# Optimization experiments

Measured on AMD Instinct MI355X. Metric: run time of the kernel, lower is better.

## Reference

```python
import jax, jax.numpy as jnp
import numpy as np

N = 200_000          # active voxels
CIN, COUT = 64, 128  # in_filters, out_filters
GRID = (32, 480, 480)  # sparse spatial shape (D, H, W)
NEG_SLOPE = 0.01     # nn.LeakyReLU default
EPS = 1e-5           # BatchNorm1d default


def _build_nbrs():
    """Build rulebook-style neighbor tables for the two submanifold kernels.

    Returns nbr31 [9, N] for kernel (3,1,3) and nbr13 [9, N] for kernel (1,3,3).
    Entry == N means 'no active neighbor' (maps to a zero pad row).
    """
    rng = np.random.default_rng(0)
    prod = GRID[0] * GRID[1] * GRID[2]
    lin = rng.choice(prod, size=N, replace=False)
    z, y, x = np.unravel_index(lin, GRID)
    lut = np.full(prod, N, dtype=np.int64)
    lut[lin] = np.arange(N)

    def nbrs(offsets):
        out = np.full((len(offsets), N), N, dtype=np.int32)
        for k, (dz, dy, dx) in enumerate(offsets):
            zz, yy, xx = z + dz, y + dy, x + dx
            valid = ((zz >= 0) & (zz < GRID[0]) & (yy >= 0) & (yy < GRID[1])
                     & (xx >= 0) & (xx < GRID[2]))
            l2 = (zz * GRID[1] + yy) * GRID[2] + xx
            out[k, valid] = lut[l2[valid]].astype(np.int32)
        return out

    off31 = [(dz, 0, dx) for dz in (-1, 0, 1) for dx in (-1, 0, 1)]  # (3,1,3)
    off13 = [(0, dy, dx) for dy in (-1, 0, 1) for dx in (-1, 0, 1)]  # (1,3,3)
    return nbrs(off31), nbrs(off13)


def setup_inputs() -> dict:
    key = jax.random.key(0)
    ks = jax.random.split(key, 5)
    nbr31, nbr13 = _build_nbrs()
    s_in = (2.0 / (9 * CIN)) ** 0.5
    s_out = (2.0 / (9 * COUT)) ** 0.5
    ones = jnp.ones((COUT,), jnp.float32)
    zeros = jnp.zeros((COUT,), jnp.float32)
    return {
        "feats": jax.random.normal(ks[0], (N, CIN), jnp.float32),
        "W1": jax.random.normal(ks[1], (9, CIN, COUT), jnp.float32) * s_in,
        "W1_2": jax.random.normal(ks[2], (9, COUT, COUT), jnp.float32) * s_out,
        "W2": jax.random.normal(ks[3], (9, CIN, COUT), jnp.float32) * s_in,
        "W3": jax.random.normal(ks[4], (9, COUT, COUT), jnp.float32) * s_out,
        "g0": ones, "b0": zeros,      # bn0  (init: weight=1, bias=0)
        "g0_2": ones, "b0_2": zeros,  # bn0_2
        "g1": ones, "b1": zeros,      # bn1
        "g2": ones, "b2": zeros,      # bn2
        "nbr31": jnp.asarray(nbr31),
        "nbr13": jnp.asarray(nbr13),
    }


def _subm_conv(f, W, nbr):
    # f [N, Cin], W [9, Cin, Cout], nbr [9, N] -> [N, Cout]
    fp = jnp.concatenate([f, jnp.zeros((1, f.shape[1]), f.dtype)], axis=0)
    g = fp[nbr]  # gather: [9, N, Cin]
    return jnp.einsum("knc,kcd->nd", g, W)


def _lrelu(f):
    return jnp.where(f >= 0, f, NEG_SLOPE * f)


def _bn(f, gamma, beta):
    # BatchNorm1d training-mode batch stats (biased variance) over voxel dim
    m = jnp.mean(f, axis=0)
    v = jnp.mean(jnp.square(f), axis=0) - m * m
    return (f - m) * jax.lax.rsqrt(v + EPS) * gamma + beta


def reference(feats, W1, W1_2, W2, W3, g0, b0, g0_2, b0_2, g1, b1, g2, b2,
              nbr31, nbr13):
    shortcut = _bn(_lrelu(_subm_conv(feats, W1, nbr31)), g0, b0)
    shortcut = _bn(_lrelu(_subm_conv(shortcut, W1_2, nbr13)), g0_2, b0_2)
    resA = _bn(_lrelu(_subm_conv(feats, W2, nbr13)), g1, b1)
    resA = _bn(_lrelu(_subm_conv(resA, W3, nbr31)), g2, b2)
    return resA + shortcut
```

## Files before the change

kernel.cpp:

```cpp
#include <hip/hip_runtime.h>

#define NV 200000
#define NCH 782
#define PCAP 32
#define CG 3125
#define PN 3907
#define RB1 123

typedef __attribute__((ext_vector_type(8))) short sh8;
typedef __attribute__((ext_vector_type(4))) float f32x4;
typedef __attribute__((ext_vector_type(2))) unsigned int u32x2;

__device__ inline unsigned short f2bf(float f) {
  unsigned int u = __builtin_bit_cast(unsigned int, f);
  u += 0x7FFFu + ((u >> 16) & 1u);
  return (unsigned short)(u >> 16);
}
__device__ inline float bf2f(unsigned short h) {
  unsigned int u = ((unsigned int)h) << 16;
  return __builtin_bit_cast(float, u);
}
__device__ inline float lrelu(float v) { return v >= 0.f ? v : 0.01f * v; }

__global__ __launch_bounds__(256) void prep_k(
    const float* __restrict__ W1, const float* __restrict__ W12,
    const float* __restrict__ W2, const float* __restrict__ W3,
    unsigned short* __restrict__ T1, unsigned short* __restrict__ T12,
    unsigned short* __restrict__ T2, unsigned short* __restrict__ T3,
    const int* __restrict__ nbr31, const int* __restrict__ nbr13,
    int2* __restrict__ pairs, int* __restrict__ cc) {
  __shared__ unsigned short lt[64 * 130];
  __shared__ int base_s[4];
  int bx = blockIdx.x;
  const int tid = threadIdx.x;
  if (bx < 36) {
    const float* src;
    unsigned short* dst;
    int cin, k;
    if (bx < 9) { src = W1; dst = T1; cin = 64; k = bx; }
    else if (bx < 18) { src = W2; dst = T2; cin = 64; k = bx - 9; }
    else if (bx < 27) { src = W12; dst = T12; cin = 128; k = bx - 18; }
    else { src = W3; dst = T3; cin = 128; k = bx - 27; }
    src += (size_t)k * cin * 128;
    dst += (size_t)k * 128 * cin;
    const int cmask = cin - 1;
    const int csh = (cin == 64) ? 6 : 7;
    for (int h = 0; h < 2; ++h) {
      if (h) __syncthreads();
      const int tot = cin * 64;
      for (int e = tid; e < tot; e += 256) {
        const int c = e >> 6, dd = e & 63;
        lt[dd * 130 + c] = f2bf(src[c * 128 + h * 64 + dd]);
      }
      __syncthreads();
      for (int o = tid; o < tot; o += 256) {
        const int dl = o >> csh, c = o & cmask;
        dst[(size_t)(h * 64 + dl) * cin + c] = lt[dl * 130 + c];
      }
    }
    return;
  }
  bx -= 36;
  const int slot = bx / NCH, chunk = bx % NCH;
  const int table = slot >> 3, kk = slot & 7;
  const int k = kk + (kk >= 4);
  const int* nb = (table ? nbr13 : nbr31) + (size_t)k * NV;
  const int lane = tid & 63, wv = tid >> 6;
  const int n = chunk * 256 + tid;
  const int val = (n < NV) ? nb[n] : NV;
  const bool valid = (val != NV);
  const unsigned long long m = __ballot(valid);
  const int loff = __popcll(m & ((1ull << lane) - 1ull));
  if (lane == 0) base_s[wv] = __popcll(m);
  __syncthreads();
  int wbase = 0;
  for (int w = 0; w < wv; ++w) wbase += base_s[w];
  int2* pw = pairs + (size_t)(slot * NCH + chunk) * PCAP;
  if (valid) {
    const int pos = wbase + loff;
    if (pos < PCAP) {
      int2 pr;
      pr.x = val;
      pr.y = n;
      pw[pos] = pr;
    }
  }
  if (tid == 0) {
    const int tot = base_s[0] + base_s[1] + base_s[2] + base_s[3];
    cc[slot * NCH + chunk] = min(tot, PCAP);
  }
}

#define STATS_EMIT(ACC, PART, PROW)                                             \
  {                                                                             \
    f32x4 ssum[2], ssq[2];                                                      \
    _Pragma("unroll") for (int mt = 0; mt < 2; ++mt) {                          \
      ssum[mt] = (f32x4){0.f, 0.f, 0.f, 0.f};                                   \
      ssq[mt] = (f32x4){0.f, 0.f, 0.f, 0.f};                                    \
      _Pragma("unroll") for (int nt = 0; nt < 4; ++nt)                          \
          _Pragma("unroll") for (int q = 0; q < 4; ++q) {                       \
        const float f = lrelu(ACC[mt][nt][q]);                                  \
        ssum[mt][q] += f;                                                       \
        ssq[mt][q] += f * f;                                                    \
      }                                                                         \
      _Pragma("unroll") for (int off = 1; off < 16; off <<= 1)                  \
          _Pragma("unroll") for (int q = 0; q < 4; ++q) {                       \
        ssum[mt][q] += __shfl_xor(ssum[mt][q], off);                            \
        ssq[mt][q] += __shfl_xor(ssq[mt][q], off);                              \
      }                                                                         \
      if (l15 == 0) {                                                           \
        const int d0 = (wv * 2 + mt) * 16 + l4 * 4;                             \
        *(f32x4*)(PART + (size_t)(PROW)*256 + d0) = ssum[mt];                   \
        *(f32x4*)(PART + (size_t)(PROW)*256 + 128 + d0) = ssq[mt];              \
      }                                                                         \
    }                                                                           \
  }

#define TILE_OUT(ACC, YPTR)                                                     \
  {                                                                             \
    __syncthreads();                                                            \
    _Pragma("unroll") for (int mt = 0; mt < 2; ++mt)                            \
        _Pragma("unroll") for (int nt = 0; nt < 4; ++nt) {                      \
      u32x2 pk;                                                                 \
      pk[0] = (unsigned)f2bf(ACC[mt][nt][0]) |                                  \
              ((unsigned)f2bf(ACC[mt][nt][1]) << 16);                           \
      pk[1] = (unsigned)f2bf(ACC[mt][nt][2]) |                                  \
              ((unsigned)f2bf(ACC[mt][nt][3]) << 16);                           \
      *(u32x2*)(&lds[(nt * 16 + l15) * 136 + (wv * 2 + mt) * 16 + l4 * 4]) = pk;\
    }                                                                           \
    __syncthreads();                                                            \
    _Pragma("unroll") for (int j = 0; j < 4; ++j) {                             \
      const int row = j * 16 + (tid >> 4);                                      \
      const int c16 = tid & 15;                                                 \
      const sh8 v = *(const sh8*)(&lds[row * 136 + c16 * 8]);                   \
      *(sh8*)(YPTR + (size_t)(row0 + row) * 128 + c16 * 8) = v;                 \
    }                                                                           \
  }

__global__ __launch_bounds__(256) void center2_k(
    const float* __restrict__ X, const unsigned short* __restrict__ W1t,
    const unsigned short* __restrict__ W2t, unsigned short* __restrict__ Y1,
    unsigned short* __restrict__ Y2, float* __restrict__ PA,
    float* __restrict__ PB) {
  constexpr int CIN = 64, CH = 8;
  __shared__ unsigned short lds[64 * 136];
  const int tid = threadIdx.x, lane = tid & 63, wv = tid >> 6;
  const int l15 = lane & 15, l4 = lane >> 4;
  const int prow = blockIdx.x;
  const int row0 = prow * 64;
  const int js = tid & 7;
#pragma unroll
  for (int i = 0; i < 2; ++i) {
    const int r = (i * 256 + tid) >> 3;
    const f32x4 a = *(const f32x4*)(X + (size_t)(row0 + r) * CIN + js * 8);
    const f32x4 b = *(const f32x4*)(X + (size_t)(row0 + r) * CIN + js * 8 + 4);
    sh8 o;
#pragma unroll
    for (int j = 0; j < 4; ++j) {
      o[j] = (short)f2bf(a[j]);
      o[4 + j] = (short)f2bf(b[j]);
    }
    *(sh8*)(lds + ((size_t)r * CH + (js ^ (r & 7))) * 8) = o;
  }
  __syncthreads();

  f32x4 acc1[2][4], acc2[2][4];
#pragma unroll
  for (int mt = 0; mt < 2; ++mt)
#pragma unroll
    for (int nt = 0; nt < 4; ++nt) {
      acc1[mt][nt] = (f32x4){0.f, 0.f, 0.f, 0.f};
      acc2[mt][nt] = (f32x4){0.f, 0.f, 0.f, 0.f};
    }
  const unsigned short* W1K = W1t + (size_t)(4 * 128) * CIN;
  const unsigned short* W2K = W2t + (size_t)(4 * 128) * CIN;
#pragma unroll
  for (int s = 0; s < 2; ++s) {
    sh8 aw1[2], aw2[2];
#pragma unroll
    for (int mt = 0; mt < 2; ++mt) {
      const int d = (wv * 2 + mt) * 16 + l15;
      aw1[mt] = *(const sh8*)(W1K + (size_t)d * CIN + s * 32 + l4 * 8);
      aw2[mt] = *(const sh8*)(W2K + (size_t)d * CIN + s * 32 + l4 * 8);
    }
#pragma unroll
    for (int nt = 0; nt < 4; ++nt) {
      const int r = nt * 16 + l15;
      const int j = s * 4 + l4;
      const sh8 bx = *(const sh8*)(lds + ((size_t)r * CH + (j ^ (r & 7))) * 8);
#pragma unroll
      for (int mt = 0; mt < 2; ++mt) {
        acc1[mt][nt] =
            __builtin_amdgcn_mfma_f32_16x16x32_bf16(aw1[mt], bx, acc1[mt][nt], 0, 0, 0);
        acc2[mt][nt] =
            __builtin_amdgcn_mfma_f32_16x16x32_bf16(aw2[mt], bx, acc2[mt][nt], 0, 0, 0);
      }
    }
  }
  STATS_EMIT(acc1, PA, prow)
  STATS_EMIT(acc2, PB, prow)
  TILE_OUT(acc1, Y1)
  __syncthreads();
  TILE_OUT(acc2, Y2)
}

__global__ __launch_bounds__(256) void c128m_k(
    const unsigned short* __restrict__ y1, const unsigned short* __restrict__ y2,
    const unsigned short* __restrict__ T12, const unsigned short* __restrict__ T3,
    const float* __restrict__ ab, unsigned short* __restrict__ ysc,
    unsigned short* __restrict__ y3, float* __restrict__ PA,
    float* __restrict__ PB) {
  constexpr int CIN = 128, CH = 16;
  __shared__ unsigned short lds[64 * 136];
  const int bx = blockIdx.x;
  const bool first = bx < CG;
  const unsigned short* X = first ? y1 : y2;
  const unsigned short* Wt = first ? T12 : T3;
  const float* abp = first ? ab : ab + 256;
  unsigned short* Y = first ? ysc : y3;
  float* PART = first ? PA : PB;
  const int prow = first ? bx : bx - CG;
  const int row0 = prow * 64;
  const int tid = threadIdx.x, lane = tid & 63, wv = tid >> 6;
  const int l15 = lane & 15, l4 = lane >> 4;
  const int js = tid & 15;
  const f32x4 aL = *(const f32x4*)(abp + js * 8);
  const f32x4 aH = *(const f32x4*)(abp + js * 8 + 4);
  const f32x4 bL = *(const f32x4*)(abp + 128 + js * 8);
  const f32x4 bH = *(const f32x4*)(abp + 128 + js * 8 + 4);
#pragma unroll
  for (int i = 0; i < 4; ++i) {
    const int r = (i * 256 + tid) >> 4;
    const sh8 v = *(const sh8*)(X + (size_t)(row0 + r) * CIN + js * 8);
    sh8 o;
#pragma unroll
    for (int j = 0; j < 4; ++j) {
      o[j] = (short)f2bf(lrelu(bf2f((unsigned short)v[j])) * aL[j] + bL[j]);
      o[4 + j] = (short)f2bf(lrelu(bf2f((unsigned short)v[4 + j])) * aH[j] + bH[j]);
    }
    *(sh8*)(lds + ((size_t)r * CH + (js ^ (r & 7))) * 8) = o;
  }
  __syncthreads();

  f32x4 acc[2][4];
#pragma unroll
  for (int mt = 0; mt < 2; ++mt)
#pragma unroll
    for (int nt = 0; nt < 4; ++nt) acc[mt][nt] = (f32x4){0.f, 0.f, 0.f, 0.f};

  const unsigned short* WtK = Wt + (size_t)(4 * 128) * CIN;
#pragma unroll
  for (int s = 0; s < 4; ++s) {
    sh8 aw[2];
#pragma unroll
    for (int mt = 0; mt < 2; ++mt) {
      const int d = (wv * 2 + mt) * 16 + l15;
      aw[mt] = *(const sh8*)(WtK + (size_t)d * CIN + s * 32 + l4 * 8);
    }
#pragma unroll
    for (int nt = 0; nt < 4; ++nt) {
      const int r = nt * 16 + l15;
      const int j = s * 4 + l4;
      const sh8 bxv = *(const sh8*)(lds + ((size_t)r * CH + (j ^ (r & 7))) * 8);
#pragma unroll
      for (int mt = 0; mt < 2; ++mt)
        acc[mt][nt] =
            __builtin_amdgcn_mfma_f32_16x16x32_bf16(aw[mt], bxv, acc[mt][nt], 0, 0, 0);
    }
  }
  STATS_EMIT(acc, PART, prow)
  TILE_OUT(acc, Y)
}

__global__ __launch_bounds__(256) void off64_k(
    const float* __restrict__ X, const unsigned short* __restrict__ T1,
    const unsigned short* __restrict__ T2, const int2* __restrict__ pairs,
    const int* __restrict__ cc, unsigned short* __restrict__ y1,
    unsigned short* __restrict__ y2, float* __restrict__ PA,
    float* __restrict__ PB) {
  constexpr int CIN = 64, CH = 8;
  const int layer = blockIdx.x / NCH, chunk = blockIdx.x % NCH;
  const unsigned short* Wt = layer ? T2 : T1;
  unsigned short* Y = layer ? y2 : y1;
  float* PD = layer ? PB : PA;
  const int* ccl = cc + layer * 8 * NCH;
  const int2* pl = pairs + (size_t)layer * 8 * NCH * PCAP;
  __shared__ unsigned short tile[32 * CIN];
  __shared__ int sin[32], sout[32];
  const int tid = threadIdx.x, lane = tid & 63, wv = tid >> 6;
  const int l15 = lane & 15, l4 = lane >> 4;
  const int js = tid & 7;
  const int sr = tid >> 3;
  f32x4 ds[2], dq[2];
#pragma unroll
  for (int mt = 0; mt < 2; ++mt) {
    ds[mt] = (f32x4){0.f, 0.f, 0.f, 0.f};
    dq[mt] = (f32x4){0.f, 0.f, 0.f, 0.f};
  }

  for (int kk = 0; kk < 8; ++kk) {
    const int n0 = ccl[kk * NCH + chunk];
    if (n0 == 0) continue;
    const int k = kk + (kk >= 4);
    const unsigned short* WtK = Wt + (size_t)k * 128 * CIN;
    __syncthreads();
    if (tid < 32) {
      int2 pr;
      if (tid < n0) pr = pl[(size_t)(kk * NCH + chunk) * PCAP + tid];
      else { pr.x = NV; pr.y = NV; }
      sin[tid] = pr.x;
      sout[tid] = pr.y;
    }
    __syncthreads();
    {
      const int in = sin[sr];
      sh8 o = (sh8){0, 0, 0, 0, 0, 0, 0, 0};
      if (in != NV) {
        const f32x4 a = *(const f32x4*)(X + (size_t)in * CIN + js * 8);
        const f32x4 b = *(const f32x4*)(X + (size_t)in * CIN + js * 8 + 4);
#pragma unroll
        for (int j = 0; j < 4; ++j) {
          o[j] = (short)f2bf(a[j]);
          o[4 + j] = (short)f2bf(b[j]);
        }
      }
      *(sh8*)(tile + ((size_t)sr * CH + (js ^ (sr & 7))) * 8) = o;
    }
    __syncthreads();

    f32x4 acc[2][2];
#pragma unroll
    for (int mt = 0; mt < 2; ++mt)
#pragma unroll
      for (int nt = 0; nt < 2; ++nt) acc[mt][nt] = (f32x4){0.f, 0.f, 0.f, 0.f};
#pragma unroll
    for (int s = 0; s < 2; ++s) {
      sh8 aw[2];
#pragma unroll
      for (int mt = 0; mt < 2; ++mt) {
        const int d = (wv * 2 + mt) * 16 + l15;
        aw[mt] = *(const sh8*)(WtK + (size_t)d * CIN + s * 32 + l4 * 8);
      }
#pragma unroll
      for (int nt = 0; nt < 2; ++nt) {
        const int r = nt * 16 + l15;
        const int j = s * 4 + l4;
        const sh8 bxv = *(const sh8*)(tile + ((size_t)r * CH + (j ^ (r & 7))) * 8);
#pragma unroll
        for (int mt = 0; mt < 2; ++mt)
          acc[mt][nt] =
              __builtin_amdgcn_mfma_f32_16x16x32_bf16(aw[mt], bxv, acc[mt][nt], 0, 0, 0);
      }
    }
#pragma unroll
    for (int mt = 0; mt < 2; ++mt)
#pragma unroll
      for (int nt = 0; nt < 2; ++nt) {
        const int out = sout[nt * 16 + l15];
        if (out == NV) continue;
        const int d0 = (wv * 2 + mt) * 16 + l4 * 4;
        unsigned short* p = Y + (size_t)out * 128 + d0;
        const u32x2 old = *(const u32x2*)p;
        u32x2 nw;
        float of[4], sf[4];
        of[0] = bf2f((unsigned short)(old[0] & 0xffff));
        of[1] = bf2f((unsigned short)(old[0] >> 16));
        of[2] = bf2f((unsigned short)(old[1] & 0xffff));
        of[3] = bf2f((unsigned short)(old[1] >> 16));
#pragma unroll
        for (int q = 0; q < 4; ++q) {
          sf[q] = of[q] + acc[mt][nt][q];
          const float ln = lrelu(sf[q]), lo = lrelu(of[q]);
          ds[mt][q] += ln - lo;
          dq[mt][q] += ln * ln - lo * lo;
        }
        nw[0] = (unsigned)f2bf(sf[0]) | ((unsigned)f2bf(sf[1]) << 16);
        nw[1] = (unsigned)f2bf(sf[2]) | ((unsigned)f2bf(sf[3]) << 16);
        *(u32x2*)p = nw;
      }
  }
#pragma unroll
  for (int mt = 0; mt < 2; ++mt) {
#pragma unroll
    for (int off = 1; off < 16; off <<= 1)
#pragma unroll
      for (int q = 0; q < 4; ++q) {
        ds[mt][q] += __shfl_xor(ds[mt][q], off);
        dq[mt][q] += __shfl_xor(dq[mt][q], off);
      }
    if (l15 == 0) {
      const int d0 = (wv * 2 + mt) * 16 + l4 * 4;
      *(f32x4*)(PD + (size_t)(CG + chunk) * 256 + d0) = ds[mt];
      *(f32x4*)(PD + (size_t)(CG + chunk) * 256 + 128 + d0) = dq[mt];
    }
  }
}

__global__ __launch_bounds__(256) void off128m_k(
    const unsigned short* __restrict__ y1, const unsigned short* __restrict__ y2,
    const unsigned short* __restrict__ T12, const unsigned short* __restrict__ T3,
    const int2* __restrict__ pairs, const int* __restrict__ cc,
    const float* __restrict__ ab, unsigned short* __restrict__ ysc,
    unsigned short* __restrict__ y3, float* __restrict__ PA,
    float* __restrict__ PB) {
  constexpr int CIN = 128, CH = 16;
  const int lay = blockIdx.x / NCH, chunk = blockIdx.x % NCH;
  const unsigned short* X = lay ? y2 : y1;
  const unsigned short* Wt = lay ? T3 : T12;
  const float* abp = lay ? ab + 256 : ab;
  unsigned short* Y = lay ? y3 : ysc;
  float* PD = lay ? PB : PA;
  const int2* pt = pairs + (lay ? 0 : (size_t)8 * NCH * PCAP);
  const int* ct = cc + (lay ? 0 : 8 * NCH);
  __shared__ unsigned short tile[32 * CIN];
  __shared__ int sin[32], sout[32];
  const int tid = threadIdx.x, lane = tid & 63, wv = tid >> 6;
  const int l15 = lane & 15, l4 = lane >> 4;
  const int js = tid & 15;
  const f32x4 aL = *(const f32x4*)(abp + js * 8);
  const f32x4 aH = *(const f32x4*)(abp + js * 8 + 4);
  const f32x4 bL = *(const f32x4*)(abp + 128 + js * 8);
  const f32x4 bH = *(const f32x4*)(abp + 128 + js * 8 + 4);
  f32x4 ds[2], dq[2];
#pragma unroll
  for (int mt = 0; mt < 2; ++mt) {
    ds[mt] = (f32x4){0.f, 0.f, 0.f, 0.f};
    dq[mt] = (f32x4){0.f, 0.f, 0.f, 0.f};
  }

  for (int kk = 0; kk < 8; ++kk) {
    const int n0 = ct[kk * NCH + chunk];
    if (n0 == 0) continue;
    const int k = kk + (kk >= 4);
    const unsigned short* WtK = Wt + (size_t)k * 128 * CIN;
    __syncthreads();
    if (tid < 32) {
      int2 pr;
      if (tid < n0) pr = pt[(size_t)(kk * NCH + chunk) * PCAP + tid];
      else { pr.x = NV; pr.y = NV; }
      sin[tid] = pr.x;
      sout[tid] = pr.y;
    }
    __syncthreads();
#pragma unroll
    for (int i = 0; i < 2; ++i) {
      const int r = (i * 256 + tid) >> 4;
      const int in = sin[r];
      sh8 o = (sh8){0, 0, 0, 0, 0, 0, 0, 0};
      if (in != NV) {
        const sh8 v = *(const sh8*)(X + (size_t)in * CIN + js * 8);
#pragma unroll
        for (int j = 0; j < 4; ++j) {
          o[j] = (short)f2bf(lrelu(bf2f((unsigned short)v[j])) * aL[j] + bL[j]);
          o[4 + j] = (short)f2bf(lrelu(bf2f((unsigned short)v[4 + j])) * aH[j] + bH[j]);
        }
      }
      *(sh8*)(tile + ((size_t)r * CH + (js ^ (r & 7))) * 8) = o;
    }
    __syncthreads();

    f32x4 acc[2][2];
#pragma unroll
    for (int mt = 0; mt < 2; ++mt)
#pragma unroll
      for (int nt = 0; nt < 2; ++nt) acc[mt][nt] = (f32x4){0.f, 0.f, 0.f, 0.f};
#pragma unroll
    for (int s = 0; s < 4; ++s) {
      sh8 aw[2];
#pragma unroll
      for (int mt = 0; mt < 2; ++mt) {
        const int d = (wv * 2 + mt) * 16 + l15;
        aw[mt] = *(const sh8*)(WtK + (size_t)d * CIN + s * 32 + l4 * 8);
      }
#pragma unroll
      for (int nt = 0; nt < 2; ++nt) {
        const int r = nt * 16 + l15;
        const int j = s * 4 + l4;
        const sh8 bxv = *(const sh8*)(tile + ((size_t)r * CH + (j ^ (r & 7))) * 8);
#pragma unroll
        for (int mt = 0; mt < 2; ++mt)
          acc[mt][nt] =
              __builtin_amdgcn_mfma_f32_16x16x32_bf16(aw[mt], bxv, acc[mt][nt], 0, 0, 0);
      }
    }
#pragma unroll
    for (int mt = 0; mt < 2; ++mt)
#pragma unroll
      for (int nt = 0; nt < 2; ++nt) {
        const int out = sout[nt * 16 + l15];
        if (out == NV) continue;
        const int d0 = (wv * 2 + mt) * 16 + l4 * 4;
        unsigned short* p = Y + (size_t)out * 128 + d0;
        const u32x2 old = *(const u32x2*)p;
        u32x2 nw;
        float of[4], sf[4];
        of[0] = bf2f((unsigned short)(old[0] & 0xffff));
        of[1] = bf2f((unsigned short)(old[0] >> 16));
        of[2] = bf2f((unsigned short)(old[1] & 0xffff));
        of[3] = bf2f((unsigned short)(old[1] >> 16));
#pragma unroll
        for (int q = 0; q < 4; ++q) {
          sf[q] = of[q] + acc[mt][nt][q];
          const float ln = lrelu(sf[q]), lo = lrelu(of[q]);
          ds[mt][q] += ln - lo;
          dq[mt][q] += ln * ln - lo * lo;
        }
        nw[0] = (unsigned)f2bf(sf[0]) | ((unsigned)f2bf(sf[1]) << 16);
        nw[1] = (unsigned)f2bf(sf[2]) | ((unsigned)f2bf(sf[3]) << 16);
        *(u32x2*)p = nw;
      }
  }
#pragma unroll
  for (int mt = 0; mt < 2; ++mt) {
#pragma unroll
    for (int off = 1; off < 16; off <<= 1)
#pragma unroll
      for (int q = 0; q < 4; ++q) {
        ds[mt][q] += __shfl_xor(ds[mt][q], off);
        dq[mt][q] += __shfl_xor(dq[mt][q], off);
      }
    if (l15 == 0) {
      const int d0 = (wv * 2 + mt) * 16 + l4 * 4;
      *(f32x4*)(PD + (size_t)(CG + chunk) * 256 + d0) = ds[mt];
      *(f32x4*)(PD + (size_t)(CG + chunk) * 256 + 128 + d0) = dq[mt];
    }
  }
}

__global__ __launch_bounds__(256) void red1_k(const float* __restrict__ PA,
                                              const float* __restrict__ PB,
                                              float* __restrict__ RA,
                                              float* __restrict__ RB) {
  const int tb = blockIdx.x / RB1;
  const int b = blockIdx.x % RB1;
  const float* P = tb ? PB : PA;
  float* R = tb ? RB : RA;
  const int c = threadIdx.x;
  const int r0 = b * 32;
  const int r1 = (r0 + 32 < PN) ? r0 + 32 : PN;
  float s = 0.f;
#pragma unroll 4
  for (int r = r0; r < r1; ++r) s += P[(size_t)r * 256 + c];
  R[(size_t)b * 256 + c] = s;
}

__global__ __launch_bounds__(1024) void fin2_k(
    const float* __restrict__ RA, const float* __restrict__ gA,
    const float* __restrict__ btA, float* __restrict__ abA,
    const float* __restrict__ RB, const float* __restrict__ gB,
    const float* __restrict__ btB, float* __restrict__ abB) {
  const float* R = blockIdx.x ? RB : RA;
  const float* g = blockIdx.x ? gB : gA;
  const float* bt = blockIdx.x ? btB : btA;
  float* abo = blockIdx.x ? abB : abA;
  __shared__ float S[1024];
  const int t = threadIdx.x;
  const int c = t & 255, grp = t >> 8;
  float s = 0.f;
  for (int b = grp; b < RB1; b += 4) s += R[(size_t)b * 256 + c];
  S[t] = s;
  __syncthreads();
  if (t < 256) S[t] = S[t] + S[256 + t] + S[512 + t] + S[768 + t];
  __syncthreads();
  if (t < 128) {
    const float m = S[t] * (1.0f / (float)NV);
    const float v = S[128 + t] * (1.0f / (float)NV) - m * m;
    const float a = g[t] * rsqrtf(v + 1e-5f);
    abo[t] = a;
    abo[128 + t] = bt[t] - m * a;
  }
}

__global__ __launch_bounds__(256) void final_k(const unsigned short* __restrict__ y3,
                                               const unsigned short* __restrict__ ysc,
                                               const float* __restrict__ ab3,
                                               const float* __restrict__ ab1,
                                               float* __restrict__ out) {
  const long i = (long)blockIdx.x * 256 + threadIdx.x;
  if (i >= (long)NV * 16) return;
  const long base = i * 8;
  const int c0 = (int)(base & 127);
  const sh8 v3 = *(const sh8*)(y3 + base);
  const sh8 vs = *(const sh8*)(ysc + base);
  const f32x4 a3L = *(const f32x4*)(ab3 + c0);
  const f32x4 a3H = *(const f32x4*)(ab3 + c0 + 4);
  const f32x4 b3L = *(const f32x4*)(ab3 + 128 + c0);
  const f32x4 b3H = *(const f32x4*)(ab3 + 128 + c0 + 4);
  const f32x4 a1L = *(const f32x4*)(ab1 + c0);
  const f32x4 a1H = *(const f32x4*)(ab1 + c0 + 4);
  const f32x4 b1L = *(const f32x4*)(ab1 + 128 + c0);
  const f32x4 b1H = *(const f32x4*)(ab1 + 128 + c0 + 4);
  f32x4 oL, oH;
#pragma unroll
  for (int j = 0; j < 4; ++j) {
    oL[j] = a3L[j] * lrelu(bf2f((unsigned short)v3[j])) + b3L[j] +
            a1L[j] * lrelu(bf2f((unsigned short)vs[j])) + b1L[j];
    oH[j] = a3H[j] * lrelu(bf2f((unsigned short)v3[4 + j])) + b3H[j] +
            a1H[j] * lrelu(bf2f((unsigned short)vs[4 + j])) + b1H[j];
  }
  *(f32x4*)(out + base) = oL;
  *(f32x4*)(out + base + 4) = oH;
}

extern "C" void kernel_launch(void* const* d_in, const int* in_sizes, int n_in,
                              void* d_out, int out_size, void* d_ws, size_t ws_size,
                              hipStream_t stream) {
  const float* feats = (const float*)d_in[0];
  const float* W1 = (const float*)d_in[1];
  const float* W12 = (const float*)d_in[2];
  const float* W2 = (const float*)d_in[3];
  const float* W3 = (const float*)d_in[4];
  const float* g0 = (const float*)d_in[5];
  const float* b0 = (const float*)d_in[6];
  const float* g02 = (const float*)d_in[7];
  const float* b02 = (const float*)d_in[8];
  const float* g1 = (const float*)d_in[9];
  const float* b1 = (const float*)d_in[10];
  const float* g2 = (const float*)d_in[11];
  const float* b2 = (const float*)d_in[12];
  const int* nbr31 = (const int*)d_in[13];
  const int* nbr13 = (const int*)d_in[14];
  float* out = (float*)d_out;

  char* ws = (char*)d_ws;
  size_t off = 0;
  auto alloc = [&](size_t bytes) {
    char* p = ws + off;
    off = (off + bytes + 255) & ~(size_t)255;
    return p;
  };

  unsigned short* T1 = (unsigned short*)alloc((size_t)9 * 128 * 64 * 2);
  unsigned short* T2 = (unsigned short*)alloc((size_t)9 * 128 * 64 * 2);
  unsigned short* T12 = (unsigned short*)alloc((size_t)9 * 128 * 128 * 2);
  unsigned short* T3 = (unsigned short*)alloc((size_t)9 * 128 * 128 * 2);
  unsigned short* y1 = (unsigned short*)alloc((size_t)NV * 128 * 2);
  unsigned short* y2 = (unsigned short*)alloc((size_t)NV * 128 * 2);
  unsigned short* ysc = (unsigned short*)alloc((size_t)NV * 128 * 2);
  unsigned short* y3 = (unsigned short*)alloc((size_t)NV * 128 * 2);
  float* PA = (float*)alloc((size_t)PN * 256 * 4);
  float* PB = (float*)alloc((size_t)PN * 256 * 4);
  float* RA = (float*)alloc((size_t)RB1 * 256 * 4);
  float* RB = (float*)alloc((size_t)RB1 * 256 * 4);
  float* ab = (float*)alloc(1024 * 4);
  int* cc = (int*)alloc((size_t)16 * NCH * 4);
  int2* pairs = (int2*)alloc((size_t)16 * NCH * PCAP * 8);


  prep_k<<<36 + 16 * NCH, 256, 0, stream>>>(W1, W12, W2, W3, T1, T12, T2, T3,
                                            nbr31, nbr13, pairs, cc);
  center2_k<<<CG, 256, 0, stream>>>(feats, T1, T2, y1, y2, PA, PB);
  off64_k<<<2 * NCH, 256, 0, stream>>>(feats, T1, T2, pairs, cc, y1, y2, PA, PB);
  red1_k<<<2 * RB1, 256, 0, stream>>>(PA, PB, RA, RB);
  fin2_k<<<2, 1024, 0, stream>>>(RA, g0, b0, ab + 0, RB, g1, b1, ab + 256);
  c128m_k<<<2 * CG, 256, 0, stream>>>(y1, y2, T12, T3, ab, ysc, y3, PA, PB);
  off128m_k<<<2 * NCH, 256, 0, stream>>>(y1, y2, T12, T3, pairs, cc, ab, ysc, y3,
                                         PA, PB);
  red1_k<<<2 * RB1, 256, 0, stream>>>(PA, PB, RA, RB);
  fin2_k<<<2, 1024, 0, stream>>>(RA, g02, b02, ab + 512, RB, g2, b2, ab + 768);
  final_k<<<12500, 256, 0, stream>>>(y3, ysc, ab + 768, ab + 512, out);
}
```

Measured before the change: 306.3 us.

## Double the voxel chunk per block and read pair lists directly from global

Each block now handles chunks of 512 voxels instead of 256. The pair-compaction kernel loops twice over the chunk with a running count, and the pair capacity per chunk-offset goes from 32 to 56. The off-center conv kernels use a 64-row tile with four MFMA column tiles, so each weight fragment load feeds more MMAs and half as many blocks are launched. The shared-memory staging of in/out pair indices and its extra barrier are dropped in favour of direct global reads of the pair list. The cost is more registers, more padded work when a chunk's count is low, and a changed overflow cap that could truncate pairs if a chunk has more than 56 valid neighbours.

```diff
diff --git a/kernel.cpp b/kernel.cpp
--- a/kernel.cpp
+++ b/kernel.cpp
@@ -1,11 +1,11 @@
 #include <hip/hip_runtime.h>
 
 #define NV 200000
-#define NCH 782
-#define PCAP 32
+#define NCH 391
+#define PCAP 56
 #define CG 3125
-#define PN 3907
-#define RB1 123
+#define PN 3516
+#define RB1 110
 
 typedef __attribute__((ext_vector_type(8))) short sh8;
 typedef __attribute__((ext_vector_type(4))) float f32x4;
@@ -31,6 +31,7 @@
     int2* __restrict__ pairs, int* __restrict__ cc) {
   __shared__ unsigned short lt[64 * 130];
   __shared__ int base_s[4];
+  __shared__ int run;
   int bx = blockIdx.x;
   const int tid = threadIdx.x;
   if (bx < 36) {
@@ -66,29 +67,34 @@
   const int k = kk + (kk >= 4);
   const int* nb = (table ? nbr13 : nbr31) + (size_t)k * NV;
   const int lane = tid & 63, wv = tid >> 6;
-  const int n = chunk * 256 + tid;
-  const int val = (n < NV) ? nb[n] : NV;
-  const bool valid = (val != NV);
-  const unsigned long long m = __ballot(valid);
-  const int loff = __popcll(m & ((1ull << lane) - 1ull));
-  if (lane == 0) base_s[wv] = __popcll(m);
+  if (tid == 0) run = 0;
   __syncthreads();
-  int wbase = 0;
-  for (int w = 0; w < wv; ++w) wbase += base_s[w];
   int2* pw = pairs + (size_t)(slot * NCH + chunk) * PCAP;
-  if (valid) {
-    const int pos = wbase + loff;
-    if (pos < PCAP) {
-      int2 pr;
-      pr.x = val;
-      pr.y = n;
-      pw[pos] = pr;
-    }
-  }
-  if (tid == 0) {
-    const int tot = base_s[0] + base_s[1] + base_s[2] + base_s[3];
-    cc[slot * NCH + chunk] = min(tot, PCAP);
-  }
+#pragma unroll
+  for (int i = 0; i < 2; ++i) {
+    const int n = chunk * 512 + i * 256 + tid;
+    const int val = (n < NV) ? nb[n] : NV;
+    const bool valid = (val != NV);
+    const unsigned long long m = __ballot(valid);
+    const int loff = __popcll(m & ((1ull << lane) - 1ull));
+    if (lane == 0) base_s[wv] = __popcll(m);
+    __syncthreads();
+    int wbase = run;
+    for (int w = 0; w < wv; ++w) wbase += base_s[w];
+    if (valid) {
+      const int pos = wbase + loff;
+      if (pos < PCAP) {
+        int2 pr;
+        pr.x = val;
+        pr.y = n;
+        pw[pos] = pr;
+      }
+    }
+    __syncthreads();
+    if (tid == 0) run += base_s[0] + base_s[1] + base_s[2] + base_s[3];
+    __syncthreads();
+  }
+  if (tid == 0) cc[slot * NCH + chunk] = min(run, PCAP);
 }
 
 #define STATS_EMIT(ACC, PART, PROW)                                             \
@@ -285,12 +291,10 @@
   float* PD = layer ? PB : PA;
   const int* ccl = cc + layer * 8 * NCH;
   const int2* pl = pairs + (size_t)layer * 8 * NCH * PCAP;
-  __shared__ unsigned short tile[32 * CIN];
-  __shared__ int sin[32], sout[32];
+  __shared__ unsigned short tile[64 * CIN];
   const int tid = threadIdx.x, lane = tid & 63, wv = tid >> 6;
   const int l15 = lane & 15, l4 = lane >> 4;
   const int js = tid & 7;
-  const int sr = tid >> 3;
   f32x4 ds[2], dq[2];
 #pragma unroll
   for (int mt = 0; mt < 2; ++mt) {
@@ -303,17 +307,12 @@
     if (n0 == 0) continue;
     const int k = kk + (kk >= 4);
     const unsigned short* WtK = Wt + (size_t)k * 128 * CIN;
+    const int2* pw = pl + (size_t)(kk * NCH + chunk) * PCAP;
     __syncthreads();
-    if (tid < 32) {
-      int2 pr;
-      if (tid < n0) pr = pl[(size_t)(kk * NCH + chunk) * PCAP + tid];
-      else { pr.x = NV; pr.y = NV; }
-      sin[tid] = pr.x;
-      sout[tid] = pr.y;
-    }
-    __syncthreads();
-    {
-      const int in = sin[sr];
+#pragma unroll
+    for (int i = 0; i < 2; ++i) {
+      const int r = (i * 256 + tid) >> 3;
+      const int in = (r < n0) ? pw[r].x : NV;
       sh8 o = (sh8){0, 0, 0, 0, 0, 0, 0, 0};
       if (in != NV) {
         const f32x4 a = *(const f32x4*)(X + (size_t)in * CIN + js * 8);
@@ -324,15 +323,15 @@
           o[4 + j] = (short)f2bf(b[j]);
         }
       }
-      *(sh8*)(tile + ((size_t)sr * CH + (js ^ (sr & 7))) * 8) = o;
+      *(sh8*)(tile + ((size_t)r * CH + (js ^ (r & 7))) * 8) = o;
     }
     __syncthreads();
 
-    f32x4 acc[2][2];
+    f32x4 acc[2][4];
 #pragma unroll
     for (int mt = 0; mt < 2; ++mt)
 #pragma unroll
-      for (int nt = 0; nt < 2; ++nt) acc[mt][nt] = (f32x4){0.f, 0.f, 0.f, 0.f};
+      for (int nt = 0; nt < 4; ++nt) acc[mt][nt] = (f32x4){0.f, 0.f, 0.f, 0.f};
 #pragma unroll
     for (int s = 0; s < 2; ++s) {
       sh8 aw[2];
@@ -342,7 +341,7 @@
         aw[mt] = *(const sh8*)(WtK + (size_t)d * CIN + s * 32 + l4 * 8);
       }
 #pragma unroll
-      for (int nt = 0; nt < 2; ++nt) {
+      for (int nt = 0; nt < 4; ++nt) {
         const int r = nt * 16 + l15;
         const int j = s * 4 + l4;
         const sh8 bxv = *(const sh8*)(tile + ((size_t)r * CH + (j ^ (r & 7))) * 8);
@@ -355,8 +354,9 @@
 #pragma unroll
     for (int mt = 0; mt < 2; ++mt)
 #pragma unroll
-      for (int nt = 0; nt < 2; ++nt) {
-        const int out = sout[nt * 16 + l15];
+      for (int nt = 0; nt < 4; ++nt) {
+        const int rr = nt * 16 + l15;
+        const int out = (rr < n0) ? pw[rr].y : NV;
         if (out == NV) continue;
         const int d0 = (wv * 2 + mt) * 16 + l4 * 4;
         unsigned short* p = Y + (size_t)out * 128 + d0;
@@ -412,8 +412,7 @@
   float* PD = lay ? PB : PA;
   const int2* pt = pairs + (lay ? 0 : (size_t)8 * NCH * PCAP);
   const int* ct = cc + (lay ? 0 : 8 * NCH);
-  __shared__ unsigned short tile[32 * CIN];
-  __shared__ int sin[32], sout[32];
+  __shared__ unsigned short tile[64 * CIN];
   const int tid = threadIdx.x, lane = tid & 63, wv = tid >> 6;
   const int l15 = lane & 15, l4 = lane >> 4;
   const int js = tid & 15;
@@ -433,19 +432,12 @@
     if (n0 == 0) continue;
     const int k = kk + (kk >= 4);
     const unsigned short* WtK = Wt + (size_t)k * 128 * CIN;
+    const int2* pw = pt + (size_t)(kk * NCH + chunk) * PCAP;
     __syncthreads();
-    if (tid < 32) {
-      int2 pr;
-      if (tid < n0) pr = pt[(size_t)(kk * NCH + chunk) * PCAP + tid];
-      else { pr.x = NV; pr.y = NV; }
-      sin[tid] = pr.x;
-      sout[tid] = pr.y;
-    }
-    __syncthreads();
-#pragma unroll
-    for (int i = 0; i < 2; ++i) {
+#pragma unroll
+    for (int i = 0; i < 4; ++i) {
       const int r = (i * 256 + tid) >> 4;
-      const int in = sin[r];
+      const int in = (r < n0) ? pw[r].x : NV;
       sh8 o = (sh8){0, 0, 0, 0, 0, 0, 0, 0};
       if (in != NV) {
         const sh8 v = *(const sh8*)(X + (size_t)in * CIN + js * 8);
@@ -459,11 +451,11 @@
     }
     __syncthreads();
 
-    f32x4 acc[2][2];
+    f32x4 acc[2][4];
 #pragma unroll
     for (int mt = 0; mt < 2; ++mt)
 #pragma unroll
-      for (int nt = 0; nt < 2; ++nt) acc[mt][nt] = (f32x4){0.f, 0.f, 0.f, 0.f};
+      for (int nt = 0; nt < 4; ++nt) acc[mt][nt] = (f32x4){0.f, 0.f, 0.f, 0.f};
 #pragma unroll
     for (int s = 0; s < 4; ++s) {
       sh8 aw[2];
@@ -473,7 +465,7 @@
         aw[mt] = *(const sh8*)(WtK + (size_t)d * CIN + s * 32 + l4 * 8);
       }
 #pragma unroll
-      for (int nt = 0; nt < 2; ++nt) {
+      for (int nt = 0; nt < 4; ++nt) {
         const int r = nt * 16 + l15;
         const int j = s * 4 + l4;
         const sh8 bxv = *(const sh8*)(tile + ((size_t)r * CH + (j ^ (r & 7))) * 8);
@@ -486,8 +478,9 @@
 #pragma unroll
     for (int mt = 0; mt < 2; ++mt)
 #pragma unroll
-      for (int nt = 0; nt < 2; ++nt) {
-        const int out = sout[nt * 16 + l15];
+      for (int nt = 0; nt < 4; ++nt) {
+        const int rr = nt * 16 + l15;
+        const int out = (rr < n0) ? pw[rr].y : NV;
         if (out == NV) continue;
         const int d0 = (wv * 2 + mt) * 16 + l4 * 4;
         unsigned short* p = Y + (size_t)out * 128 + d0;
```

Measured after the change: 288.0 us. -6.0%, faster.
